# Optimization experiments

Hardware: AMD Instinct MI355X
Metric: run time of the kernel (lower is better)

Reference implementation:

```python
import jax, jax.numpy as jnp
import numpy as np

H, DK, DV, S = 16, 1024, 1024, 2048
DH_QK = DK // H  # 64, per-head q/k dim
DH_V = DV // H   # 64, per-head v dim


def setup_inputs() -> dict:
    key = jax.random.key(0)
    ks = jax.random.split(key, 11)
    init = lambda k, shape, fan_in: jax.random.uniform(k, shape, jnp.float32, -1.0, 1.0) / jnp.sqrt(jnp.float32(fan_in))
    return {
        "Q": jax.random.normal(ks[0], (S, DK), jnp.float32),
        "K": jax.random.normal(ks[1], (S, DK), jnp.float32),
        "V": jax.random.normal(ks[2], (S, DV), jnp.float32),
        # per-head Linear weights, torch convention [out, in] stacked over heads
        "Wq": init(ks[3], (H, DH_QK, DH_QK), DH_QK),
        "bq": init(ks[4], (H, DH_QK), DH_QK),
        "Wk": init(ks[5], (H, DH_QK, DH_QK), DH_QK),
        "bk": init(ks[6], (H, DH_QK), DH_QK),
        "Wv": init(ks[7], (H, DH_V, DH_V), DH_V),
        "bv": init(ks[8], (H, DH_V), DH_V),
        "Wo": init(ks[9], (DK, H * DH_V), H * DH_V),  # final linear: d_model x (h*dv_h)
        "bo": init(ks[10], (DK,), H * DH_V),
    }


def reference(Q, K, V, Wq, bq, Wk, bk, Wv, bv, Wo, bo):
    h, dh = Wq.shape[0], Wq.shape[2]
    dv = Wv.shape[2]
    s = Q.shape[0]
    # split features into h per-head chunks (same as slicing loop in torch)
    Qh = Q.reshape(s, h, dh)
    Kh = K.reshape(s, h, dh)
    Vh = V.reshape(s, h, dv)
    # per-head Linear: x @ W.T + b, batched over heads
    q = jnp.einsum('shd,hed->she', Qh, Wq) + bq
    k = jnp.einsum('shd,hed->she', Kh, Wk) + bk
    v = jnp.einsum('shd,hed->she', Vh, Wv) + bv
    # scaled dot-product attention per head
    scores = jnp.einsum('she,the->hst', q, k) / jnp.sqrt(jnp.float32(dh))
    attn = jax.nn.softmax(scores, axis=-1)
    o = jnp.einsum('hst,the->she', attn, v)  # [s, h, dv]
    concat = o.reshape(s, h * dv)
    return concat @ Wo.T + bo
```

## Files before the change

### kernel.cpp

```cpp
#include <hip/hip_runtime.h>
#include <stdint.h>

static constexpr int H   = 16;
static constexpr int S   = 2048;
static constexpr int DHd = 64;
static constexpr int DM  = 1024;
static constexpr int NSPLIT = 4;
static constexpr int KT_PER_SPLIT = (S / 64) / NSPLIT;

using f32x4   = __attribute__((ext_vector_type(4))) float;
using f32x8   = __attribute__((ext_vector_type(8))) float;
using f32x16  = __attribute__((ext_vector_type(16))) float;
using short8  = __attribute__((ext_vector_type(8))) short;
using bf16x8  = __attribute__((ext_vector_type(8))) __bf16;
using uint4v  = __attribute__((ext_vector_type(4))) unsigned int;

#if __has_builtin(__builtin_amdgcn_exp2f)
#define EXP2F __builtin_amdgcn_exp2f
#else
#define EXP2F exp2f
#endif

__device__ __forceinline__ short f2bf(float f) {
  union { float f; uint32_t u; } v; v.f = f;
  uint32_t r = v.u + 0x7FFFu + ((v.u >> 16) & 1u);
  return (short)(r >> 16);
}
__device__ __forceinline__ float bf2f(short s) {
  union { uint32_t u; float f; } v;
  v.u = ((uint32_t)(unsigned short)s) << 16;
  return v.f;
}

__device__ __forceinline__ short8 f2bf8(f32x4 a, f32x4 b) {
  short8 v;
  v[0] = f2bf(a[0]); v[1] = f2bf(a[1]); v[2] = f2bf(a[2]); v[3] = f2bf(a[3]);
  v[4] = f2bf(b[0]); v[5] = f2bf(b[1]); v[6] = f2bf(b[2]); v[7] = f2bf(b[3]);
  return v;
}

__device__ __forceinline__ unsigned int pkbf(float a, float b) {
  __bf16 x = (__bf16)a, y = (__bf16)b;
  unsigned short ux = __builtin_bit_cast(unsigned short, x);
  unsigned short uy = __builtin_bit_cast(unsigned short, y);
  return (unsigned int)ux | ((unsigned int)uy << 16);
}

__device__ __forceinline__ f32x4 mfma16(short8 a, short8 b, f32x4 c) {
  return __builtin_amdgcn_mfma_f32_16x16x32_bf16(
      __builtin_bit_cast(bf16x8, a), __builtin_bit_cast(bf16x8, b), c, 0, 0, 0);
}
__device__ __forceinline__ f32x16 mfma32(short8 a, short8 b, f32x16 c) {
  return __builtin_amdgcn_mfma_f32_32x32x16_bf16(
      __builtin_bit_cast(bf16x8, a), __builtin_bit_cast(bf16x8, b), c, 0, 0, 0);
}

__device__ __forceinline__ short8 lds_read_swz(const short* base, int row, int chunk) {
  return *(const short8*)((const char*)base + row * 128 + ((chunk ^ (row & 7)) << 4));
}
__device__ __forceinline__ void lds_write_swz(short* base, int row, int chunk, short8 v) {
  *(short8*)((char*)base + row * 128 + ((chunk ^ (row & 7)) << 4)) = v;
}

using u32g = __attribute__((address_space(1))) const unsigned int;
using u32l = __attribute__((address_space(3))) unsigned int;
__device__ __forceinline__ void gl_lds16(const short* g, short* l) {
  __builtin_amdgcn_global_load_lds(
      reinterpret_cast<u32g*>(reinterpret_cast<uintptr_t>(g)),
      reinterpret_cast<u32l*>(static_cast<unsigned int>(reinterpret_cast<uintptr_t>(l))),
      16, 0, 0);
}

__global__ __launch_bounds__(256) void proj_kernel(
    const float* __restrict__ Q, const float* __restrict__ K, const float* __restrict__ V,
    const float* __restrict__ Wq, const float* __restrict__ bq,
    const float* __restrict__ Wk, const float* __restrict__ bk,
    const float* __restrict__ Wv, const float* __restrict__ bv,
    short* __restrict__ qb, short* __restrict__ kb, short* __restrict__ vtb) {
  const int h    = blockIdx.y;
  const int rt   = blockIdx.x * 128;
  const int mode = blockIdx.z;

  const float* X; const float* W; const float* bias;
  if (mode == 0)      { X = Q; W = Wq; bias = bq; }
  else if (mode == 1) { X = K; W = Wk; bias = bk; }
  else                { X = V; W = Wv; bias = bv; }
  bias += h * DHd;
  const float scale = (mode == 0) ? 0.125f * 1.44269504f : 1.0f;

  __shared__ short Xs[128 * 64];
  __shared__ short Ws[64 * 64];
  __shared__ short Ot[64 * 136];

  const int t = threadIdx.x;

#pragma unroll
  for (int p = 0; p < 4; p++) {
    int ci = p * 256 + t;
    int row = ci >> 3, oct = ci & 7;
    const float* g = X + (size_t)(rt + row) * DM + h * DHd + oct * 8;
    f32x4 x0 = *(const f32x4*)g;
    f32x4 x1 = *(const f32x4*)(g + 4);
    lds_write_swz(Xs, row, oct, f2bf8(x0, x1));
  }
#pragma unroll
  for (int p = 0; p < 2; p++) {
    int ci = p * 256 + t;
    int row = ci >> 3, oct = ci & 7;
    const float* g = W + (size_t)h * DHd * DHd + row * DHd + oct * 8;
    f32x4 x0 = *(const f32x4*)g;
    f32x4 x1 = *(const f32x4*)(g + 4);
    lds_write_swz(Ws, row, oct, f2bf8(x0, x1));
  }
  __syncthreads();

  const int wid = t >> 6, lane = t & 63;
  const int l15 = lane & 15, l4 = lane >> 4;

  f32x4 acc[2][4] = {};
#pragma unroll
  for (int ks = 0; ks < 2; ks++) {
    int chunk = ks * 4 + l4;
    short8 a0 = lds_read_swz(Xs, wid * 32 + l15, chunk);
    short8 a1 = lds_read_swz(Xs, wid * 32 + 16 + l15, chunk);
#pragma unroll
    for (int nf = 0; nf < 4; nf++) {
      short8 b = lds_read_swz(Ws, nf * 16 + l15, chunk);
      acc[0][nf] = mfma16(a0, b, acc[0][nf]);
      acc[1][nf] = mfma16(a1, b, acc[1][nf]);
    }
  }

  if (mode < 2) {
    short* out = (mode == 0) ? qb : kb;
#pragma unroll
    for (int mf = 0; mf < 2; mf++)
#pragma unroll
      for (int nf = 0; nf < 4; nf++) {
        int col = nf * 16 + l15;
        float b = bias[col];
#pragma unroll
        for (int r = 0; r < 4; r++) {
          int row = rt + wid * 32 + mf * 16 + l4 * 4 + r;
          out[((size_t)h * S + row) * DHd + col] = f2bf((acc[mf][nf][r] + b) * scale);
        }
      }
  } else {
#pragma unroll
    for (int mf = 0; mf < 2; mf++)
#pragma unroll
      for (int nf = 0; nf < 4; nf++) {
        int col = nf * 16 + l15;
        float b = bias[col];
#pragma unroll
        for (int r = 0; r < 4; r++) {
          int lrow = wid * 32 + mf * 16 + l4 * 4 + r;
          Ot[col * 136 + lrow] = f2bf(acc[mf][nf][r] + b);
        }
      }
    __syncthreads();
#pragma unroll
    for (int p = 0; p < 4; p++) {
      int ci = p * 256 + t;
      int e = ci >> 4, c8 = ci & 15;
      short8 v = *(const short8*)&Ot[e * 136 + c8 * 8];
      *(short8*)(vtb + ((size_t)h * DHd + e) * S + rt + c8 * 8) = v;
    }
  }
}

__global__ __launch_bounds__(256) void cvt_wo(const float* __restrict__ Wo,
                                              short* __restrict__ wob) {
  int i = (blockIdx.x * 256 + threadIdx.x) * 8;
  f32x4 x0 = *(const f32x4*)(Wo + i);
  f32x4 x1 = *(const f32x4*)(Wo + i + 4);
  *(short8*)(wob + i) = f2bf8(x0, x1);
}

__global__ __launch_bounds__(256, 2) void attn_kernel(
    const short* __restrict__ qb, const short* __restrict__ kb,
    const short* __restrict__ vtb, short* __restrict__ OpT,
    float* __restrict__ lbuf) {
  const int h  = blockIdx.y;
  const int sp = blockIdx.z;
  const int t = threadIdx.x, wid = t >> 6, lane = t & 63;
  const int l31 = lane & 31, l5 = lane >> 5;
  const int qw = blockIdx.x * 256 + wid * 64;

  __shared__ short Ks[2][64 * 64];
  __shared__ short Vs[2][64 * 64];

  short8 qf[2][4];
#pragma unroll
  for (int tt = 0; tt < 2; tt++) {
    const short* qrow = qb + ((size_t)h * S + qw + tt * 32 + l31) * DHd;
#pragma unroll
    for (int c = 0; c < 4; c++) qf[tt][c] = *(const short8*)(qrow + c * 16 + l5 * 8);
  }

  const int srow8 = lane >> 3, schunk = lane & 7;
  const int r0 = wid * 16 + srow8, r1 = r0 + 8;
  const int kt0 = sp * KT_PER_SPLIT;
  const short* kg0 = kb + ((size_t)h * S + (size_t)kt0 * 64 + r0) * DHd + ((schunk ^ (r0 & 7)) * 8);
  const short* kg1 = kb + ((size_t)h * S + (size_t)kt0 * 64 + r1) * DHd + ((schunk ^ (r1 & 7)) * 8);
  const short* vg0 = vtb + ((size_t)h * DHd + r0) * S + (size_t)kt0 * 64 + ((schunk ^ (r0 & 7)) * 8);
  const short* vg1 = vtb + ((size_t)h * DHd + r1) * S + (size_t)kt0 * 64 + ((schunk ^ (r1 & 7)) * 8);

  auto stage = [&](int buf, int kk) {
    const size_t ka = (size_t)kk * 64 * DHd;
    const size_t va = (size_t)kk * 64;
    gl_lds16(kg0 + ka, &Ks[buf][wid * 1024]);
    gl_lds16(kg1 + ka, &Ks[buf][wid * 1024 + 512]);
    gl_lds16(vg0 + va, &Vs[buf][wid * 1024]);
    gl_lds16(vg1 + va, &Vs[buf][wid * 1024 + 512]);
  };

  stage(0, 0);
  asm volatile("s_waitcnt vmcnt(0)" ::: "memory");
  __syncthreads();

  f32x16 oa00 = {}, oa01 = {}, oa10 = {}, oa11 = {};
  f32x8 lac0 = {}, lac1 = {};

  for (int kk = 0; kk < KT_PER_SPLIT; kk++) {
    const int cur = kk & 1;
    if (kk + 1 < KT_PER_SPLIT) stage(cur ^ 1, kk + 1);

    f32x16 s00 = {}, s01 = {}, s10 = {}, s11 = {};
    __builtin_amdgcn_s_setprio(1);
#pragma unroll
    for (int c = 0; c < 4; c++) {
      short8 ak0 = lds_read_swz(Ks[cur], l31, 2 * c + l5);
      short8 ak1 = lds_read_swz(Ks[cur], 32 + l31, 2 * c + l5);
      s00 = mfma32(ak0, qf[0][c], s00);
      s01 = mfma32(ak1, qf[0][c], s01);
      s10 = mfma32(ak0, qf[1][c], s10);
      s11 = mfma32(ak1, qf[1][c], s11);
    }
    __builtin_amdgcn_s_setprio(0);

#pragma unroll
    for (int i = 0; i < 16; i++) {
      float p00 = EXP2F(s00[i]), p01 = EXP2F(s01[i]);
      float p10 = EXP2F(s10[i]), p11 = EXP2F(s11[i]);
      s00[i] = p00; s01[i] = p01; s10[i] = p10; s11[i] = p11;
      lac0[i & 7] += p00 + p01;
      lac1[i & 7] += p10 + p11;
    }

    unsigned int pk0[2][8], pk1[2][8];
#pragma unroll
    for (int g = 0; g < 4; g++) {
      pk0[0][g * 2 + 0] = pkbf(s00[4 * g + 0], s00[4 * g + 1]);
      pk0[0][g * 2 + 1] = pkbf(s00[4 * g + 2], s00[4 * g + 3]);
      pk0[1][g * 2 + 0] = pkbf(s01[4 * g + 0], s01[4 * g + 1]);
      pk0[1][g * 2 + 1] = pkbf(s01[4 * g + 2], s01[4 * g + 3]);
      pk1[0][g * 2 + 0] = pkbf(s10[4 * g + 0], s10[4 * g + 1]);
      pk1[0][g * 2 + 1] = pkbf(s10[4 * g + 2], s10[4 * g + 3]);
      pk1[1][g * 2 + 0] = pkbf(s11[4 * g + 0], s11[4 * g + 1]);
      pk1[1][g * 2 + 1] = pkbf(s11[4 * g + 2], s11[4 * g + 3]);
    }

    __builtin_amdgcn_s_setprio(1);
#pragma unroll
    for (int j = 0; j < 4; j++) {
      const int bb = j >> 1;
      const int g2 = (j & 1) * 4;
      short8 av0 = lds_read_swz(Vs[cur], l31, 2 * j + l5);
      short8 av1 = lds_read_swz(Vs[cur], 32 + l31, 2 * j + l5);
#pragma unroll
      for (int tt = 0; tt < 2; tt++) {
        unsigned int (*pk)[8] = tt ? pk1 : pk0;
        unsigned int a0 = pk[bb][g2 + 0], a1 = pk[bb][g2 + 1];
        unsigned int b0 = pk[bb][g2 + 2], b1 = pk[bb][g2 + 3];
        unsigned int s0 = l5 ? a0 : b0, s1 = l5 ? a1 : b1;
        unsigned int r0x = (unsigned int)__shfl_xor((int)s0, 32);
        unsigned int r1x = (unsigned int)__shfl_xor((int)s1, 32);
        unsigned int w0 = l5 ? b0 : a0, w1 = l5 ? b1 : a1;
        uint4v pf;
        pf[0] = l5 ? r0x : w0; pf[1] = l5 ? r1x : w1;
        pf[2] = l5 ? w0 : r0x; pf[3] = l5 ? w1 : r1x;
        short8 pfrag = __builtin_bit_cast(short8, pf);
        if (tt == 0) {
          oa00 = mfma32(av0, pfrag, oa00);
          oa01 = mfma32(av1, pfrag, oa01);
        } else {
          oa10 = mfma32(av0, pfrag, oa10);
          oa11 = mfma32(av1, pfrag, oa11);
        }
      }
    }
    __builtin_amdgcn_s_setprio(0);

    asm volatile("s_waitcnt vmcnt(0)" ::: "memory");
    __syncthreads();
  }

#pragma unroll
  for (int st = 4; st >= 1; st >>= 1)
#pragma unroll
    for (int i = 0; i < st; i++) { lac0[i] += lac0[i + st]; lac1[i] += lac1[i + st]; }
  float l0 = lac0[0] + __shfl_xor(lac0[0], 32);
  float l1 = lac1[0] + __shfl_xor(lac1[0], 32);

#pragma unroll
  for (int r = 0; r < 16; r++) {
    int dvb = (r & 3) + 8 * (r >> 2) + 4 * l5;
    size_t base = (((size_t)sp * H + h) * DHd + dvb) * S + qw + l31;
    OpT[base]            = f2bf(oa00[r]);
    OpT[base + 32UL * S] = f2bf(oa01[r]);
    OpT[base + 32]            = f2bf(oa10[r]);
    OpT[base + 32UL * S + 32] = f2bf(oa11[r]);
  }
  if (l5 == 0) {
    lbuf[((size_t)sp * H + h) * S + qw + l31]      = l0;
    lbuf[((size_t)sp * H + h) * S + qw + 32 + l31] = l1;
  }
}

__global__ __launch_bounds__(256) void combine_kernel(
    const short* __restrict__ OpT, const float* __restrict__ lbuf,
    short* __restrict__ Ob) {
  const int h  = blockIdx.y;
  const int s0 = blockIdx.x * 64;
  __shared__ short tile[64][72];

  const int t = threadIdx.x;
  const int sl = t & 63, dvg = t >> 6;
  const int s = s0 + sl;

  float lt = 0.f;
#pragma unroll
  for (int sp = 0; sp < NSPLIT; sp++)
    lt += lbuf[((size_t)sp * H + h) * S + s];
  float inv = 1.0f / lt;

  float val[16];
#pragma unroll
  for (int p = 0; p < 16; p++) {
    int dv = dvg * 16 + p;
    float o = 0.f;
#pragma unroll
    for (int sp = 0; sp < NSPLIT; sp++)
      o += bf2f(OpT[(((size_t)sp * H + h) * DHd + dv) * S + s]);
    val[p] = o * inv;
  }
  short8 v0, v1;
#pragma unroll
  for (int i = 0; i < 8; i++) { v0[i] = f2bf(val[i]); v1[i] = f2bf(val[8 + i]); }
  *(short8*)&tile[sl][dvg * 16]     = v0;
  *(short8*)&tile[sl][dvg * 16 + 8] = v1;
  __syncthreads();

#pragma unroll
  for (int i = 0; i < 2; i++) {
    int cid = t + i * 256;
    int r = cid >> 3, c = cid & 7;
    short8 v = *(const short8*)&tile[r][c * 8];
    *(short8*)(Ob + (size_t)(s0 + r) * DM + h * DHd + c * 8) = v;
  }
}

__global__ __launch_bounds__(256) void out_gemm(
    const short* __restrict__ Ob, const short* __restrict__ wob,
    const float* __restrict__ bo, float* __restrict__ out) {
  const int m0 = blockIdx.x * 64;
  const int n0 = blockIdx.y * 64;

  __shared__ short As[2][64 * 64];
  __shared__ short Bs[2][64 * 64];

  const int t = threadIdx.x, wid = t >> 6, lane = t & 63;
  const int l15 = lane & 15, l4 = lane >> 4;
  const int srow8 = lane >> 3, schunk = lane & 7;
  const int r0 = wid * 16 + srow8, r1 = r0 + 8;

  const short* ag0 = Ob  + (size_t)(m0 + r0) * DM + ((schunk ^ (r0 & 7)) * 8);
  const short* ag1 = Ob  + (size_t)(m0 + r1) * DM + ((schunk ^ (r1 & 7)) * 8);
  const short* bg0 = wob + (size_t)(n0 + r0) * DM + ((schunk ^ (r0 & 7)) * 8);
  const short* bg1 = wob + (size_t)(n0 + r1) * DM + ((schunk ^ (r1 & 7)) * 8);

  auto stage = [&](int buf, int kc) {
    const int off = kc * 64;
    gl_lds16(ag0 + off, &As[buf][wid * 1024]);
    gl_lds16(ag1 + off, &As[buf][wid * 1024 + 512]);
    gl_lds16(bg0 + off, &Bs[buf][wid * 1024]);
    gl_lds16(bg1 + off, &Bs[buf][wid * 1024 + 512]);
  };

  stage(0, 0);
  asm volatile("s_waitcnt vmcnt(0)" ::: "memory");
  __syncthreads();

  f32x4 acc[4] = {};
  for (int kc = 0; kc < DM / 64; kc++) {
    const int cur = kc & 1;
    if (kc + 1 < DM / 64) stage(cur ^ 1, kc + 1);
#pragma unroll
    for (int ks = 0; ks < 2; ks++) {
      int chunk = ks * 4 + l4;
      short8 a = lds_read_swz(As[cur], wid * 16 + l15, chunk);
#pragma unroll
      for (int nf = 0; nf < 4; nf++) {
        short8 b = lds_read_swz(Bs[cur], nf * 16 + l15, chunk);
        acc[nf] = mfma16(a, b, acc[nf]);
      }
    }
    asm volatile("s_waitcnt vmcnt(0)" ::: "memory");
    __syncthreads();
  }
#pragma unroll
  for (int nf = 0; nf < 4; nf++) {
    int col = n0 + nf * 16 + l15;
    float b = bo[col];
#pragma unroll
    for (int r = 0; r < 4; r++) {
      int row = m0 + wid * 16 + l4 * 4 + r;
      out[(size_t)row * DM + col] = acc[nf][r] + b;
    }
  }
}

extern "C" void kernel_launch(void* const* d_in, const int* in_sizes, int n_in,
                              void* d_out, int out_size, void* d_ws, size_t ws_size,
                              hipStream_t stream) {
  const float* Q  = (const float*)d_in[0];
  const float* K  = (const float*)d_in[1];
  const float* V  = (const float*)d_in[2];
  const float* Wq = (const float*)d_in[3];
  const float* bq = (const float*)d_in[4];
  const float* Wk = (const float*)d_in[5];
  const float* bk = (const float*)d_in[6];
  const float* Wv = (const float*)d_in[7];
  const float* bv = (const float*)d_in[8];
  const float* Wo = (const float*)d_in[9];
  const float* bo = (const float*)d_in[10];

  char* ws = (char*)d_ws;
  short* qb   = (short*)(ws);
  short* kb   = (short*)(ws + ((size_t)4 << 20));
  short* vtb  = (short*)(ws + ((size_t)8 << 20));
  short* Obf  = (short*)(ws + ((size_t)12 << 20));
  short* wob  = (short*)(ws + ((size_t)16 << 20));
  short* OpT  = (short*)(ws + ((size_t)18 << 20));
  float* lbuf = (float*)(ws + ((size_t)34 << 20));

  proj_kernel<<<dim3(S / 128, H, 3), 256, 0, stream>>>(Q, K, V, Wq, bq, Wk, bk, Wv, bv,
                                                       qb, kb, vtb);
  cvt_wo<<<dim3((DM * DM) / (256 * 8)), 256, 0, stream>>>(Wo, wob);
  attn_kernel<<<dim3(S / 256, H, NSPLIT), 256, 0, stream>>>(qb, kb, vtb, OpT, lbuf);
  combine_kernel<<<dim3(S / 64, H), 256, 0, stream>>>(OpT, lbuf, Obf);
  out_gemm<<<dim3(S / 64, DM / 64), 256, 0, stream>>>(Obf, wob, bo, (float*)d_out);
}
```

Measured before the change: 56.24 us.

## Fold Wo conversion into projection kernel and permute V layout to drop P shuffles

Merges the Wo fp32-to-bf16 conversion into the projection kernel as an extra grid slice, which removes one kernel launch. It also changes how the transposed V is written so each 16-element key group is interleaved in halves. That lets the attention kernel feed packed P values directly into the PV MFMA without the cross-half lane shuffles and selects. The V-layout permutation must match the K ordering used in the P fragment, so any mismatch would silently corrupt results.

Result: faster. 52.09 us (-7.4%).

```diff
diff --git a/kernel.cpp b/kernel.cpp
--- a/kernel.cpp
+++ b/kernel.cpp
@@ -76,10 +76,25 @@
     const float* __restrict__ Wq, const float* __restrict__ bq,
     const float* __restrict__ Wk, const float* __restrict__ bk,
     const float* __restrict__ Wv, const float* __restrict__ bv,
+    const float* __restrict__ Wo, short* __restrict__ wob,
     short* __restrict__ qb, short* __restrict__ kb, short* __restrict__ vtb) {
-  const int h    = blockIdx.y;
-  const int rt   = blockIdx.x * 128;
+  const int t = threadIdx.x;
   const int mode = blockIdx.z;
+
+  if (mode == 3) {
+    int chunk = blockIdx.y * gridDim.x + blockIdx.x;
+    int i = (chunk * 256 + t) * 16;
+    f32x4 x0 = *(const f32x4*)(Wo + i);
+    f32x4 x1 = *(const f32x4*)(Wo + i + 4);
+    f32x4 x2 = *(const f32x4*)(Wo + i + 8);
+    f32x4 x3 = *(const f32x4*)(Wo + i + 12);
+    *(short8*)(wob + i)     = f2bf8(x0, x1);
+    *(short8*)(wob + i + 8) = f2bf8(x2, x3);
+    return;
+  }
+
+  const int h  = blockIdx.y;
+  const int rt = blockIdx.x * 128;
 
   const float* X; const float* W; const float* bias;
   if (mode == 0)      { X = Q; W = Wq; bias = bq; }
@@ -91,8 +106,6 @@
   __shared__ short Xs[128 * 64];
   __shared__ short Ws[64 * 64];
   __shared__ short Ot[64 * 136];
-
-  const int t = threadIdx.x;
 
 #pragma unroll
   for (int p = 0; p < 4; p++) {
@@ -160,21 +173,21 @@
       }
     __syncthreads();
 #pragma unroll
-    for (int p = 0; p < 4; p++) {
+    for (int p = 0; p < 2; p++) {
       int ci = p * 256 + t;
-      int e = ci >> 4, c8 = ci & 15;
-      short8 v = *(const short8*)&Ot[e * 136 + c8 * 8];
-      *(short8*)(vtb + ((size_t)h * DHd + e) * S + rt + c8 * 8) = v;
-    }
-  }
-}
-
-__global__ __launch_bounds__(256) void cvt_wo(const float* __restrict__ Wo,
-                                              short* __restrict__ wob) {
-  int i = (blockIdx.x * 256 + threadIdx.x) * 8;
-  f32x4 x0 = *(const f32x4*)(Wo + i);
-  f32x4 x1 = *(const f32x4*)(Wo + i + 4);
-  *(short8*)(wob + i) = f2bf8(x0, x1);
+      int e = ci >> 3, c16 = ci & 7;
+      short8 a = *(const short8*)&Ot[e * 136 + c16 * 16];
+      short8 b = *(const short8*)&Ot[e * 136 + c16 * 16 + 8];
+      short8 lo, hi;
+      lo[0] = a[0]; lo[1] = a[1]; lo[2] = a[2]; lo[3] = a[3];
+      lo[4] = b[0]; lo[5] = b[1]; lo[6] = b[2]; lo[7] = b[3];
+      hi[0] = a[4]; hi[1] = a[5]; hi[2] = a[6]; hi[3] = a[7];
+      hi[4] = b[4]; hi[5] = b[5]; hi[6] = b[6]; hi[7] = b[7];
+      short* dst = vtb + ((size_t)h * DHd + e) * S + rt + c16 * 16;
+      *(short8*)dst       = lo;
+      *(short8*)(dst + 8) = hi;
+    }
+  }
 }
 
 __global__ __launch_bounds__(256, 2) void attn_kernel(
@@ -265,30 +278,20 @@
 #pragma unroll
     for (int j = 0; j < 4; j++) {
       const int bb = j >> 1;
-      const int g2 = (j & 1) * 4;
+      const int s4 = (j & 1) * 4;
       short8 av0 = lds_read_swz(Vs[cur], l31, 2 * j + l5);
       short8 av1 = lds_read_swz(Vs[cur], 32 + l31, 2 * j + l5);
-#pragma unroll
-      for (int tt = 0; tt < 2; tt++) {
-        unsigned int (*pk)[8] = tt ? pk1 : pk0;
-        unsigned int a0 = pk[bb][g2 + 0], a1 = pk[bb][g2 + 1];
-        unsigned int b0 = pk[bb][g2 + 2], b1 = pk[bb][g2 + 3];
-        unsigned int s0 = l5 ? a0 : b0, s1 = l5 ? a1 : b1;
-        unsigned int r0x = (unsigned int)__shfl_xor((int)s0, 32);
-        unsigned int r1x = (unsigned int)__shfl_xor((int)s1, 32);
-        unsigned int w0 = l5 ? b0 : a0, w1 = l5 ? b1 : a1;
-        uint4v pf;
-        pf[0] = l5 ? r0x : w0; pf[1] = l5 ? r1x : w1;
-        pf[2] = l5 ? w0 : r0x; pf[3] = l5 ? w1 : r1x;
-        short8 pfrag = __builtin_bit_cast(short8, pf);
-        if (tt == 0) {
-          oa00 = mfma32(av0, pfrag, oa00);
-          oa01 = mfma32(av1, pfrag, oa01);
-        } else {
-          oa10 = mfma32(av0, pfrag, oa10);
-          oa11 = mfma32(av1, pfrag, oa11);
-        }
-      }
+      uint4v pf0, pf1;
+      pf0[0] = pk0[bb][s4 + 0]; pf0[1] = pk0[bb][s4 + 1];
+      pf0[2] = pk0[bb][s4 + 2]; pf0[3] = pk0[bb][s4 + 3];
+      pf1[0] = pk1[bb][s4 + 0]; pf1[1] = pk1[bb][s4 + 1];
+      pf1[2] = pk1[bb][s4 + 2]; pf1[3] = pk1[bb][s4 + 3];
+      short8 p0 = __builtin_bit_cast(short8, pf0);
+      short8 p1 = __builtin_bit_cast(short8, pf1);
+      oa00 = mfma32(av0, p0, oa00);
+      oa01 = mfma32(av1, p0, oa01);
+      oa10 = mfma32(av0, p1, oa10);
+      oa11 = mfma32(av1, p1, oa11);
     }
     __builtin_amdgcn_s_setprio(0);
 
@@ -445,9 +448,8 @@
   short* OpT  = (short*)(ws + ((size_t)18 << 20));
   float* lbuf = (float*)(ws + ((size_t)34 << 20));
 
-  proj_kernel<<<dim3(S / 128, H, 3), 256, 0, stream>>>(Q, K, V, Wq, bq, Wk, bk, Wv, bv,
-                                                       qb, kb, vtb);
-  cvt_wo<<<dim3((DM * DM) / (256 * 8)), 256, 0, stream>>>(Wo, wob);
+  proj_kernel<<<dim3(S / 128, H, 4), 256, 0, stream>>>(Q, K, V, Wq, bq, Wk, bk, Wv, bv,
+                                                       Wo, wob, qb, kb, vtb);
   attn_kernel<<<dim3(S / 256, H, NSPLIT), 256, 0, stream>>>(qb, kb, vtb, OpT, lbuf);
   combine_kernel<<<dim3(S / 64, H), 256, 0, stream>>>(OpT, lbuf, Obf);
   out_gemm<<<dim3(S / 64, DM / 64), 256, 0, stream>>>(Obf, wob, bo, (float*)d_out);
```
